# Performance work log

Hardware: AMD Instinct MI355X
Metric: run time of the kernel (lower is better)

Reference implementation:

```python
import jax, jax.numpy as jnp
import numpy as np

PI_APPROX = 3.14  # the original module uses 3.14, not math.pi
FPS = 30.0        # hard-coded sampling rate in calc_hr_torch


def setup_inputs() -> dict:
    key = jax.random.key(0)
    x = jax.random.normal(key, (4096, 4096), dtype=jnp.float32)
    return {"x": x}


def reference(x) -> jnp.ndarray:
    test_n, sig_length = x.shape
    # mean-subtract each signal (over last dim)
    x = x - jnp.mean(x, axis=-1, keepdims=True)

    # custom_fft: DFT over dim 0 (size test_n), O(N^2) via trig matmuls
    N = test_n
    n = jnp.arange(N, dtype=jnp.float32)[:, None]  # [N,1]
    k = jnp.arange(N, dtype=jnp.float32)[None, :]  # [1,N]
    ang = (-2.0 * PI_APPROX / N) * (k * n)         # [N,N]
    real_part = jnp.matmul(jnp.cos(ang), x)        # [N, sig_length]
    imag_part = jnp.matmul(jnp.sin(ang), x)

    # custom_rfft: keep non-negative frequencies along dim 0
    half = N // 2 + 1 if N % 2 == 0 else (N + 1) // 2
    real_part = real_part[:half]
    imag_part = imag_part[:half]

    Ns = sig_length
    freq = jnp.arange(Ns, dtype=jnp.float32) / (Ns / FPS)  # [sig_length]
    amplitude = jnp.sqrt(real_part ** 2 + imag_part ** 2) / Ns  # [half, sig_length]
    hr_list = freq[jnp.argmax(amplitude, axis=-1)] * 60.0       # [half]
    return hr_list
```

## Files before the change

### kernel.cpp

```cpp
#include <hip/hip_runtime.h>
#include <cmath>

typedef _Float16 f16;
typedef _Float16 f16x8 __attribute__((ext_vector_type(8)));
typedef float f32x4 __attribute__((ext_vector_type(4)));
typedef unsigned long long u64;

#define M_OUT 2049
#define NDIM 4096
#define MPAD 2112
#define CW ((float)(-2.0 * 3.14 / 4096.0))

static const size_t WS_MEAN  = 0;
static const size_t WS_CELLS = 16384;
static const size_t WS_TBL   = 40960;
static const size_t A_ELEMS  = (size_t)MPAD * NDIM;
static const size_t X_ELEMS  = (size_t)NDIM * NDIM;
static const size_t WS_XTBL  = WS_TBL + 4 * A_ELEMS * sizeof(f16);
static const size_t WS_FULL_END = WS_XTBL + 2 * X_ELEMS * sizeof(f16);
static const size_t WS_MID_END  = WS_TBL + 4 * A_ELEMS * sizeof(f16);

__device__ __forceinline__ void split_f16(float v, f16& hi, f16& lo) {
    hi = (f16)v;
    lo = (f16)((v - (float)hi) * 64.0f);
}

__global__ void mean_kernel(const float* __restrict__ x, float* __restrict__ meanv) {
    const int row = blockIdx.x;
    const float4* xr = (const float4*)(x + (size_t)row * NDIM);
    float s = 0.f;
    for (int i = threadIdx.x; i < NDIM / 4; i += 256) {
        float4 v = xr[i];
        s += (v.x + v.y) + (v.z + v.w);
    }
    for (int off = 32; off; off >>= 1) s += __shfl_down(s, off);
    __shared__ float ps[4];
    if ((threadIdx.x & 63) == 0) ps[threadIdx.x >> 6] = s;
    __syncthreads();
    if (threadIdx.x == 0) {
        float t = (ps[0] + ps[1]) + (ps[2] + ps[3]);
        meanv[row] = t * (1.0f / 4096.0f);
    }
}

__global__ void init_cells(u64* __restrict__ cells) {
    int i = blockIdx.x * 256 + threadIdx.x;
    if (i < M_OUT) cells[i] = 0ull;
}

__global__ void fill_A_cm(f16* __restrict__ tbl) {
    const int c = blockIdx.x;
    const int m = blockIdx.y * 256 + threadIdx.x;
    if (m >= MPAD) return;
    const bool valid = (m < M_OUT);
    f16x8 chv, clv, shv, slv;
    for (int j = 0; j < 8; ++j) {
        float cc = 0.f, ss = 0.f;
        if (valid) {
            int kk = c * 8 + j;
            float ang = CW * (float)(m * kk);
            sincosf(ang, &ss, &cc);
        }
        f16 h, l;
        split_f16(cc, h, l); chv[j] = h; clv[j] = l;
        split_f16(ss, h, l); shv[j] = h; slv[j] = l;
    }
    size_t idx = ((size_t)c * MPAD + m) * 8;
    *(f16x8*)(tbl + idx)                 = chv;
    *(f16x8*)(tbl + A_ELEMS + idx)       = clv;
    *(f16x8*)(tbl + 2 * A_ELEMS + idx)   = shv;
    *(f16x8*)(tbl + 3 * A_ELEMS + idx)   = slv;
}

__global__ void fill_X_cm(const float* __restrict__ x, const float* __restrict__ meanv,
                          f16* __restrict__ xtbl) {
    const int c = blockIdx.x;
    const int n = blockIdx.y * 256 + threadIdx.x;
    f16x8 hv, lv;
    for (int j = 0; j < 8; ++j) {
        int k = c * 8 + j;
        float v = x[(size_t)k * NDIM + n] - meanv[k];
        f16 h, l;
        split_f16(v, h, l);
        hv[j] = h; lv[j] = l;
    }
    size_t idx = ((size_t)c * NDIM + n) * 8;
    *(f16x8*)(xtbl + idx)           = hv;
    *(f16x8*)(xtbl + X_ELEMS + idx) = lv;
}

__global__ __launch_bounds__(256, 2) void dft_gemm_rs(
    const f16* __restrict__ atbl, const f16* __restrict__ xtbl,
    u64* __restrict__ cells)
{
    __shared__ alignas(16) f16 sX0[2][4][128][8];
    __shared__ alignas(16) f16 sX1[2][4][128][8];

    const int t = threadIdx.x;
    const int n0      = blockIdx.x * 128;
    const int rowBase = blockIdx.y * 64;

    const int lane = t & 63;
    const int w  = t >> 6;
    const int wm = w >> 1, wn = w & 1;
    const int q  = lane >> 4, ln = lane & 15;

    f32x4 aC0[2][4], aC1[2][4], aS0[2][4], aS1[2][4];
#pragma unroll
    for (int i = 0; i < 2; ++i)
#pragma unroll
        for (int j = 0; j < 4; ++j) {
            aC0[i][j] = (f32x4){0.f, 0.f, 0.f, 0.f};
            aC1[i][j] = (f32x4){0.f, 0.f, 0.f, 0.f};
            aS0[i][j] = (f32x4){0.f, 0.f, 0.f, 0.f};
            aS1[i][j] = (f32x4){0.f, 0.f, 0.f, 0.f};
        }

    int xtb[4], xch[4], xcol[4];
#pragma unroll
    for (int o = 0; o < 4; ++o) {
        int e = o * 256 + t;
        xtb[o] = e >> 9; xch[o] = (e >> 7) & 3; xcol[o] = e & 127;
    }

    auto loadX = [&](f16x8 (&xr)[4], int kc) {
#pragma unroll
        for (int o = 0; o < 4; ++o)
            xr[o] = *(const f16x8*)(xtbl + (size_t)xtb[o] * X_ELEMS
                     + (((size_t)(kc + xch[o]) * NDIM) + n0 + xcol[o]) * 8);
    };
    auto writeX = [&](f16x8 (&xr)[4], f16 (&dst)[2][4][128][8]) {
#pragma unroll
        for (int o = 0; o < 4; ++o)
            *(f16x8*)&dst[xtb[o]][xch[o]][xcol[o]][0] = xr[o];
    };

    const f16* aBase = atbl + ((size_t)q * MPAD + (rowBase + wm * 32 + ln)) * 8;
    auto loadA = [&](f16x8 (&dst)[2][4], int kc) {
#pragma unroll
        for (int tm = 0; tm < 2; ++tm)
#pragma unroll
            for (int tb = 0; tb < 4; ++tb)
                dst[tm][tb] = *(const f16x8*)(aBase + (size_t)tb * A_ELEMS
                              + ((size_t)kc * MPAD + tm * 16) * 8);
    };

    auto compute = [&](f16x8 (&A)[2][4], const f16 (&buf)[2][4][128][8]) {
        f16x8 bh[4], bl[4];
#pragma unroll
        for (int tn = 0; tn < 4; ++tn) {
            int nl = wn * 64 + tn * 16 + ln;
            bh[tn] = *(const f16x8*)&buf[0][q][nl][0];
            bl[tn] = *(const f16x8*)&buf[1][q][nl][0];
        }
#pragma unroll
        for (int tm = 0; tm < 2; ++tm)
#pragma unroll
            for (int tn = 0; tn < 4; ++tn) {
                aC0[tm][tn] = __builtin_amdgcn_mfma_f32_16x16x32_f16(A[tm][0], bh[tn], aC0[tm][tn], 0, 0, 0);
                aC1[tm][tn] = __builtin_amdgcn_mfma_f32_16x16x32_f16(A[tm][0], bl[tn], aC1[tm][tn], 0, 0, 0);
                aC1[tm][tn] = __builtin_amdgcn_mfma_f32_16x16x32_f16(A[tm][1], bh[tn], aC1[tm][tn], 0, 0, 0);
                aS0[tm][tn] = __builtin_amdgcn_mfma_f32_16x16x32_f16(A[tm][2], bh[tn], aS0[tm][tn], 0, 0, 0);
                aS1[tm][tn] = __builtin_amdgcn_mfma_f32_16x16x32_f16(A[tm][2], bl[tn], aS1[tm][tn], 0, 0, 0);
                aS1[tm][tn] = __builtin_amdgcn_mfma_f32_16x16x32_f16(A[tm][3], bh[tn], aS1[tm][tn], 0, 0, 0);
            }
    };

    f16x8 xr[4];
    f16x8 Aa[2][4], Ab[2][4];
    loadX(xr, 0);
    loadA(Aa, 0);
    for (int kc = 0; kc < 512; kc += 8) {
        writeX(xr, sX0);
        __syncthreads();
        loadX(xr, (kc + 4) & 511);
        loadA(Ab, (kc + 4) & 511);
        compute(Aa, sX0);
        writeX(xr, sX1);
        __syncthreads();
        loadX(xr, (kc + 8) & 511);
        loadA(Aa, (kc + 8) & 511);
        compute(Ab, sX1);
    }

    const float inv64 = 0.015625f;
#pragma unroll
    for (int tm = 0; tm < 2; ++tm) {
#pragma unroll
        for (int r = 0; r < 4; ++r) {
            u64 best = 0ull;
#pragma unroll
            for (int tn = 0; tn < 4; ++tn) {
                float C = aC0[tm][tn][r] + aC1[tm][tn][r] * inv64;
                float S = aS0[tm][tn][r] + aS1[tm][tn][r] * inv64;
                float a2 = C * C + S * S;
                int col = n0 + wn * 64 + tn * 16 + ln;
                u64 key = ((u64)__float_as_uint(a2) << 32) | (unsigned)(~col);
                if (key > best) best = key;
            }
            for (int off = 1; off < 16; off <<= 1) {
                unsigned hi = (unsigned)(best >> 32), lo = (unsigned)best;
                unsigned ho = __shfl_xor(hi, off);
                unsigned lo2 = __shfl_xor(lo, off);
                u64 o = ((u64)ho << 32) | lo2;
                if (o > best) best = o;
            }
            if (ln == 0) {
                int grow = rowBase + wm * 32 + tm * 16 + q * 4 + r;
                if (grow < M_OUT) atomicMax(cells + grow, best);
            }
        }
    }
}

__global__ void fill_tables_rm(f16* __restrict__ tbl) {
    long long g = (long long)blockIdx.x * 256 + threadIdx.x;
    if (g >= (long long)(MPAD * 512)) return;
    int m  = (int)(g >> 9);
    int kq = ((int)g & 511) * 8;
    bool valid = (m < M_OUT);
    f16x8 chv, clv, shv, slv;
    for (int j = 0; j < 8; ++j) {
        float c = 0.f, s = 0.f;
        if (valid) {
            int kk = kq + j;
            float ang = CW * (float)(m * kk);
            sincosf(ang, &s, &c);
        }
        f16 h, l;
        split_f16(c, h, l); chv[j] = h; clv[j] = l;
        split_f16(s, h, l); shv[j] = h; slv[j] = l;
    }
    size_t idx = (size_t)m * NDIM + kq;
    *(f16x8*)(tbl + idx)               = chv;
    *(f16x8*)(tbl + A_ELEMS + idx)     = clv;
    *(f16x8*)(tbl + 2 * A_ELEMS + idx) = shv;
    *(f16x8*)(tbl + 3 * A_ELEMS + idx) = slv;
}

#define PK 40
__global__ __launch_bounds__(256, 2) void dft_gemm_fb(
    const float* __restrict__ x, const float* __restrict__ meanv,
    const f16* __restrict__ tbl, int useTbl,
    u64* __restrict__ cells)
{
    __shared__ alignas(16) f16 Ach[64][PK];
    __shared__ alignas(16) f16 Acl[64][PK];
    __shared__ alignas(16) f16 Ash[64][PK];
    __shared__ alignas(16) f16 Asl[64][PK];
    __shared__ alignas(16) f16 Xh[128][PK];
    __shared__ alignas(16) f16 Xl[128][PK];

    const int t = threadIdx.x;
    const int n0      = blockIdx.x * 128;
    const int rowBase = blockIdx.y * 64;

    const int am  = t >> 2;
    const int akq = (t & 3) * 8;
    const int xn  = t & 127;
    const int xkh = (t >> 7) * 16;

    const int lane = t & 63;
    const int w  = t >> 6;
    const int wm = w >> 1, wn = w & 1;
    const int q  = lane >> 4, ln = lane & 15;

    f32x4 aC0[2][4], aC1[2][4], aS0[2][4], aS1[2][4];
    for (int i = 0; i < 2; ++i)
        for (int j = 0; j < 4; ++j) {
            aC0[i][j] = (f32x4){0.f, 0.f, 0.f, 0.f};
            aC1[i][j] = (f32x4){0.f, 0.f, 0.f, 0.f};
            aS0[i][j] = (f32x4){0.f, 0.f, 0.f, 0.f};
            aS1[i][j] = (f32x4){0.f, 0.f, 0.f, 0.f};
        }

    const int arow = rowBase + am;
    const bool avalid = (arow < M_OUT);

    for (int k0 = 0; k0 < NDIM; k0 += 32) {
        __syncthreads();
        if (useTbl) {
            size_t idx = (size_t)arow * NDIM + k0 + akq;
            *(f16x8*)&Ach[am][akq] = *(const f16x8*)(tbl + idx);
            *(f16x8*)&Acl[am][akq] = *(const f16x8*)(tbl + A_ELEMS + idx);
            *(f16x8*)&Ash[am][akq] = *(const f16x8*)(tbl + 2 * A_ELEMS + idx);
            *(f16x8*)&Asl[am][akq] = *(const f16x8*)(tbl + 3 * A_ELEMS + idx);
        } else {
            f16x8 chv, clv, shv, slv;
            for (int j = 0; j < 8; ++j) {
                float c = 0.f, s = 0.f;
                if (avalid) {
                    int kk = k0 + akq + j;
                    float ang = CW * (float)(arow * kk);
                    sincosf(ang, &s, &c);
                }
                f16 h, l;
                split_f16(c, h, l); chv[j] = h; clv[j] = l;
                split_f16(s, h, l); shv[j] = h; slv[j] = l;
            }
            *(f16x8*)&Ach[am][akq] = chv;
            *(f16x8*)&Acl[am][akq] = clv;
            *(f16x8*)&Ash[am][akq] = shv;
            *(f16x8*)&Asl[am][akq] = slv;
        }
        {
            const float* xp = x + (size_t)(k0 + xkh) * NDIM + n0 + xn;
            f16x8 h0, h1, l0, l1;
            for (int r = 0; r < 16; ++r) {
                float v = xp[(size_t)r * NDIM] - meanv[k0 + xkh + r];
                f16 hi, lo;
                split_f16(v, hi, lo);
                if (r < 8) { h0[r] = hi; l0[r] = lo; }
                else       { h1[r - 8] = hi; l1[r - 8] = lo; }
            }
            *(f16x8*)&Xh[xn][xkh]     = h0;
            *(f16x8*)&Xh[xn][xkh + 8] = h1;
            *(f16x8*)&Xl[xn][xkh]     = l0;
            *(f16x8*)&Xl[xn][xkh + 8] = l1;
        }
        __syncthreads();
        f16x8 fch[2], fcl[2], fsh[2], fsl[2], bh[4], bl[4];
        for (int tm = 0; tm < 2; ++tm) {
            int ml = wm * 32 + tm * 16 + ln;
            fch[tm] = *(const f16x8*)&Ach[ml][q * 8];
            fcl[tm] = *(const f16x8*)&Acl[ml][q * 8];
            fsh[tm] = *(const f16x8*)&Ash[ml][q * 8];
            fsl[tm] = *(const f16x8*)&Asl[ml][q * 8];
        }
        for (int tn = 0; tn < 4; ++tn) {
            int nl = wn * 64 + tn * 16 + ln;
            bh[tn] = *(const f16x8*)&Xh[nl][q * 8];
            bl[tn] = *(const f16x8*)&Xl[nl][q * 8];
        }
        for (int tm = 0; tm < 2; ++tm)
            for (int tn = 0; tn < 4; ++tn) {
                aC0[tm][tn] = __builtin_amdgcn_mfma_f32_16x16x32_f16(fch[tm], bh[tn], aC0[tm][tn], 0, 0, 0);
                aC1[tm][tn] = __builtin_amdgcn_mfma_f32_16x16x32_f16(fch[tm], bl[tn], aC1[tm][tn], 0, 0, 0);
                aC1[tm][tn] = __builtin_amdgcn_mfma_f32_16x16x32_f16(fcl[tm], bh[tn], aC1[tm][tn], 0, 0, 0);
                aS0[tm][tn] = __builtin_amdgcn_mfma_f32_16x16x32_f16(fsh[tm], bh[tn], aS0[tm][tn], 0, 0, 0);
                aS1[tm][tn] = __builtin_amdgcn_mfma_f32_16x16x32_f16(fsh[tm], bl[tn], aS1[tm][tn], 0, 0, 0);
                aS1[tm][tn] = __builtin_amdgcn_mfma_f32_16x16x32_f16(fsl[tm], bh[tn], aS1[tm][tn], 0, 0, 0);
            }
    }

    const float inv64 = 0.015625f;
    for (int tm = 0; tm < 2; ++tm) {
        for (int r = 0; r < 4; ++r) {
            u64 best = 0ull;
            for (int tn = 0; tn < 4; ++tn) {
                float C = aC0[tm][tn][r] + aC1[tm][tn][r] * inv64;
                float S = aS0[tm][tn][r] + aS1[tm][tn][r] * inv64;
                float a2 = C * C + S * S;
                int col = n0 + wn * 64 + tn * 16 + ln;
                u64 key = ((u64)__float_as_uint(a2) << 32) | (unsigned)(~col);
                if (key > best) best = key;
            }
            for (int off = 1; off < 16; off <<= 1) {
                unsigned hi = (unsigned)(best >> 32), lo = (unsigned)best;
                unsigned ho = __shfl_xor(hi, off);
                unsigned lo2 = __shfl_xor(lo, off);
                u64 o = ((u64)ho << 32) | lo2;
                if (o > best) best = o;
            }
            if (ln == 0) {
                int grow = rowBase + wm * 32 + tm * 16 + q * 4 + r;
                if (grow < M_OUT) atomicMax(cells + grow, best);
            }
        }
    }
}

__global__ void out_kernel(const u64* __restrict__ cells, float* __restrict__ out) {
    int i = blockIdx.x * 256 + threadIdx.x;
    if (i < M_OUT) {
        unsigned col = ~(unsigned)(cells[i] & 0xFFFFFFFFull);
        float freq = (float)col / (4096.0f / 30.0f);
        out[i] = freq * 60.0f;
    }
}

extern "C" void kernel_launch(void* const* d_in, const int* in_sizes, int n_in,
                              void* d_out, int out_size, void* d_ws, size_t ws_size,
                              hipStream_t stream) {
    const float* x = (const float*)d_in[0];
    char* ws = (char*)d_ws;
    float* meanv = (float*)(ws + WS_MEAN);
    u64*   cells = (u64*)(ws + WS_CELLS);
    f16*   atbl  = (f16*)(ws + WS_TBL);
    f16*   xtbl  = (f16*)(ws + WS_XTBL);
    float* out   = (float*)d_out;

    hipLaunchKernelGGL(init_cells, dim3((M_OUT + 255) / 256), dim3(256), 0, stream, cells);
    hipLaunchKernelGGL(mean_kernel, dim3(NDIM), dim3(256), 0, stream, x, meanv);

    if (ws_size >= WS_FULL_END) {
        hipLaunchKernelGGL(fill_A_cm, dim3(512, 9), dim3(256), 0, stream, atbl);
        hipLaunchKernelGGL(fill_X_cm, dim3(512, 16), dim3(256), 0, stream, x, meanv, xtbl);
        hipLaunchKernelGGL(dft_gemm_rs, dim3(32, 33), dim3(256), 0, stream, atbl, xtbl, cells);
    } else if (ws_size >= WS_MID_END) {
        hipLaunchKernelGGL(fill_tables_rm, dim3(4224), dim3(256), 0, stream, atbl);
        hipLaunchKernelGGL(dft_gemm_fb, dim3(32, 33), dim3(256), 0, stream,
                           x, meanv, atbl, 1, cells);
    } else {
        hipLaunchKernelGGL(dft_gemm_fb, dim3(32, 33), dim3(256), 0, stream,
                           x, meanv, atbl, 0, cells);
    }
    hipLaunchKernelGGL(out_kernel, dim3((M_OUT + 255) / 256), dim3(256), 0, stream, cells, out);
}
```

Baseline: 541.6 us.

## Switch DFT GEMM to 32x32x16 MFMA tiles and fuse setup kernels

The main GEMM now uses 32x32x16 MFMA instructions with 16-register accumulators instead of 16x16x32, which cuts LDS B-fragment reads per MFMA and changes the operand mapping and epilogue row indexing. Cell initialisation is folded into the mean kernel, and the A-table and X-table fill kernels are merged into one launch to reduce launch count. The risks are a higher accumulator register footprint and errors in the reworked lane-to-row mapping.

```diff
diff --git a/kernel.cpp b/kernel.cpp
--- a/kernel.cpp
+++ b/kernel.cpp
@@ -4,6 +4,7 @@
 typedef _Float16 f16;
 typedef _Float16 f16x8 __attribute__((ext_vector_type(8)));
 typedef float f32x4 __attribute__((ext_vector_type(4)));
+typedef float f32x16 __attribute__((ext_vector_type(16)));
 typedef unsigned long long u64;
 
 #define M_OUT 2049
@@ -25,8 +26,13 @@
     lo = (f16)((v - (float)hi) * 64.0f);
 }
 
-__global__ void mean_kernel(const float* __restrict__ x, float* __restrict__ meanv) {
+__global__ void mean_kernel(const float* __restrict__ x, float* __restrict__ meanv,
+                            u64* __restrict__ cells) {
     const int row = blockIdx.x;
+    if (blockIdx.x < 9) {
+        int ci = blockIdx.x * 256 + threadIdx.x;
+        if (ci < M_OUT) cells[ci] = 0ull;
+    }
     const float4* xr = (const float4*)(x + (size_t)row * NDIM);
     float s = 0.f;
     for (int i = threadIdx.x; i < NDIM / 4; i += 256) {
@@ -43,53 +49,48 @@
     }
 }
 
-__global__ void init_cells(u64* __restrict__ cells) {
-    int i = blockIdx.x * 256 + threadIdx.x;
-    if (i < M_OUT) cells[i] = 0ull;
-}
-
-__global__ void fill_A_cm(f16* __restrict__ tbl) {
+__global__ void fill_tables_cm(const float* __restrict__ x, const float* __restrict__ meanv,
+                               f16* __restrict__ atbl, f16* __restrict__ xtbl) {
     const int c = blockIdx.x;
-    const int m = blockIdx.y * 256 + threadIdx.x;
-    if (m >= MPAD) return;
-    const bool valid = (m < M_OUT);
-    f16x8 chv, clv, shv, slv;
-    for (int j = 0; j < 8; ++j) {
-        float cc = 0.f, ss = 0.f;
-        if (valid) {
-            int kk = c * 8 + j;
-            float ang = CW * (float)(m * kk);
-            sincosf(ang, &ss, &cc);
-        }
-        f16 h, l;
-        split_f16(cc, h, l); chv[j] = h; clv[j] = l;
-        split_f16(ss, h, l); shv[j] = h; slv[j] = l;
-    }
-    size_t idx = ((size_t)c * MPAD + m) * 8;
-    *(f16x8*)(tbl + idx)                 = chv;
-    *(f16x8*)(tbl + A_ELEMS + idx)       = clv;
-    *(f16x8*)(tbl + 2 * A_ELEMS + idx)   = shv;
-    *(f16x8*)(tbl + 3 * A_ELEMS + idx)   = slv;
-}
-
-__global__ void fill_X_cm(const float* __restrict__ x, const float* __restrict__ meanv,
-                          f16* __restrict__ xtbl) {
-    const int c = blockIdx.x;
-    const int n = blockIdx.y * 256 + threadIdx.x;
-    f16x8 hv, lv;
-    for (int j = 0; j < 8; ++j) {
-        int k = c * 8 + j;
-        float v = x[(size_t)k * NDIM + n] - meanv[k];
-        f16 h, l;
-        split_f16(v, h, l);
-        hv[j] = h; lv[j] = l;
-    }
-    size_t idx = ((size_t)c * NDIM + n) * 8;
-    *(f16x8*)(xtbl + idx)           = hv;
-    *(f16x8*)(xtbl + X_ELEMS + idx) = lv;
-}
-
-__global__ __launch_bounds__(256, 2) void dft_gemm_rs(
+    const int y = blockIdx.y;
+    if (y < 9) {
+        const int m = y * 256 + threadIdx.x;
+        if (m >= MPAD) return;
+        const bool valid = (m < M_OUT);
+        f16x8 chv, clv, shv, slv;
+        for (int j = 0; j < 8; ++j) {
+            float cc = 0.f, ss = 0.f;
+            if (valid) {
+                int kk = c * 8 + j;
+                float ang = CW * (float)(m * kk);
+                sincosf(ang, &ss, &cc);
+            }
+            f16 h, l;
+            split_f16(cc, h, l); chv[j] = h; clv[j] = l;
+            split_f16(ss, h, l); shv[j] = h; slv[j] = l;
+        }
+        size_t idx = ((size_t)c * MPAD + m) * 8;
+        *(f16x8*)(atbl + idx)                 = chv;
+        *(f16x8*)(atbl + A_ELEMS + idx)       = clv;
+        *(f16x8*)(atbl + 2 * A_ELEMS + idx)   = shv;
+        *(f16x8*)(atbl + 3 * A_ELEMS + idx)   = slv;
+    } else {
+        const int n = (y - 9) * 256 + threadIdx.x;
+        f16x8 hv, lv;
+        for (int j = 0; j < 8; ++j) {
+            int k = c * 8 + j;
+            float v = x[(size_t)k * NDIM + n] - meanv[k];
+            f16 h, l;
+            split_f16(v, h, l);
+            hv[j] = h; lv[j] = l;
+        }
+        size_t idx = ((size_t)c * NDIM + n) * 8;
+        *(f16x8*)(xtbl + idx)           = hv;
+        *(f16x8*)(xtbl + X_ELEMS + idx) = lv;
+    }
+}
+
+__global__ __launch_bounds__(256, 2) void dft_gemm_32(
     const f16* __restrict__ atbl, const f16* __restrict__ xtbl,
     u64* __restrict__ cells)
 {
@@ -103,18 +104,17 @@
     const int lane = t & 63;
     const int w  = t >> 6;
     const int wm = w >> 1, wn = w & 1;
-    const int q  = lane >> 4, ln = lane & 15;
-
-    f32x4 aC0[2][4], aC1[2][4], aS0[2][4], aS1[2][4];
-#pragma unroll
-    for (int i = 0; i < 2; ++i)
-#pragma unroll
-        for (int j = 0; j < 4; ++j) {
-            aC0[i][j] = (f32x4){0.f, 0.f, 0.f, 0.f};
-            aC1[i][j] = (f32x4){0.f, 0.f, 0.f, 0.f};
-            aS0[i][j] = (f32x4){0.f, 0.f, 0.f, 0.f};
-            aS1[i][j] = (f32x4){0.f, 0.f, 0.f, 0.f};
-        }
+    const int g  = lane >> 5;
+    const int l5 = lane & 31;
+
+    f32x16 aC0[2], aC1[2], aS0[2], aS1[2];
+#pragma unroll
+    for (int j = 0; j < 2; ++j) {
+        aC0[j] = (f32x16)(0.f);
+        aC1[j] = (f32x16)(0.f);
+        aS0[j] = (f32x16)(0.f);
+        aS1[j] = (f32x16)(0.f);
+    }
 
     int xtb[4], xch[4], xcol[4];
 #pragma unroll
@@ -122,7 +122,6 @@
         int e = o * 256 + t;
         xtb[o] = e >> 9; xch[o] = (e >> 7) & 3; xcol[o] = e & 127;
     }
-
     auto loadX = [&](f16x8 (&xr)[4], int kc) {
 #pragma unroll
         for (int o = 0; o < 4; ++o)
@@ -135,35 +134,36 @@
             *(f16x8*)&dst[xtb[o]][xch[o]][xcol[o]][0] = xr[o];
     };
 
-    const f16* aBase = atbl + ((size_t)q * MPAD + (rowBase + wm * 32 + ln)) * 8;
+    const f16* aBase = atbl + ((size_t)g * MPAD + (rowBase + wm * 32 + l5)) * 8;
     auto loadA = [&](f16x8 (&dst)[2][4], int kc) {
 #pragma unroll
-        for (int tm = 0; tm < 2; ++tm)
+        for (int s = 0; s < 2; ++s)
 #pragma unroll
             for (int tb = 0; tb < 4; ++tb)
-                dst[tm][tb] = *(const f16x8*)(aBase + (size_t)tb * A_ELEMS
-                              + ((size_t)kc * MPAD + tm * 16) * 8);
+                dst[s][tb] = *(const f16x8*)(aBase + (size_t)tb * A_ELEMS
+                              + ((size_t)(kc + 2 * s) * MPAD) * 8);
     };
 
     auto compute = [&](f16x8 (&A)[2][4], const f16 (&buf)[2][4][128][8]) {
-        f16x8 bh[4], bl[4];
-#pragma unroll
-        for (int tn = 0; tn < 4; ++tn) {
-            int nl = wn * 64 + tn * 16 + ln;
-            bh[tn] = *(const f16x8*)&buf[0][q][nl][0];
-            bl[tn] = *(const f16x8*)&buf[1][q][nl][0];
-        }
-#pragma unroll
-        for (int tm = 0; tm < 2; ++tm)
-#pragma unroll
-            for (int tn = 0; tn < 4; ++tn) {
-                aC0[tm][tn] = __builtin_amdgcn_mfma_f32_16x16x32_f16(A[tm][0], bh[tn], aC0[tm][tn], 0, 0, 0);
-                aC1[tm][tn] = __builtin_amdgcn_mfma_f32_16x16x32_f16(A[tm][0], bl[tn], aC1[tm][tn], 0, 0, 0);
-                aC1[tm][tn] = __builtin_amdgcn_mfma_f32_16x16x32_f16(A[tm][1], bh[tn], aC1[tm][tn], 0, 0, 0);
-                aS0[tm][tn] = __builtin_amdgcn_mfma_f32_16x16x32_f16(A[tm][2], bh[tn], aS0[tm][tn], 0, 0, 0);
-                aS1[tm][tn] = __builtin_amdgcn_mfma_f32_16x16x32_f16(A[tm][2], bl[tn], aS1[tm][tn], 0, 0, 0);
-                aS1[tm][tn] = __builtin_amdgcn_mfma_f32_16x16x32_f16(A[tm][3], bh[tn], aS1[tm][tn], 0, 0, 0);
-            }
+#pragma unroll
+        for (int s = 0; s < 2; ++s) {
+            f16x8 bh[2], bl[2];
+#pragma unroll
+            for (int tn = 0; tn < 2; ++tn) {
+                int nl = wn * 64 + tn * 32 + l5;
+                bh[tn] = *(const f16x8*)&buf[0][2 * s + g][nl][0];
+                bl[tn] = *(const f16x8*)&buf[1][2 * s + g][nl][0];
+            }
+#pragma unroll
+            for (int tn = 0; tn < 2; ++tn) {
+                aC0[tn] = __builtin_amdgcn_mfma_f32_32x32x16_f16(A[s][0], bh[tn], aC0[tn], 0, 0, 0);
+                aC1[tn] = __builtin_amdgcn_mfma_f32_32x32x16_f16(A[s][0], bl[tn], aC1[tn], 0, 0, 0);
+                aC1[tn] = __builtin_amdgcn_mfma_f32_32x32x16_f16(A[s][1], bh[tn], aC1[tn], 0, 0, 0);
+                aS0[tn] = __builtin_amdgcn_mfma_f32_32x32x16_f16(A[s][2], bh[tn], aS0[tn], 0, 0, 0);
+                aS1[tn] = __builtin_amdgcn_mfma_f32_32x32x16_f16(A[s][2], bl[tn], aS1[tn], 0, 0, 0);
+                aS1[tn] = __builtin_amdgcn_mfma_f32_32x32x16_f16(A[s][3], bh[tn], aS1[tn], 0, 0, 0);
+            }
+        }
     };
 
     f16x8 xr[4];
@@ -185,39 +185,36 @@
 
     const float inv64 = 0.015625f;
 #pragma unroll
-    for (int tm = 0; tm < 2; ++tm) {
-#pragma unroll
-        for (int r = 0; r < 4; ++r) {
-            u64 best = 0ull;
-#pragma unroll
-            for (int tn = 0; tn < 4; ++tn) {
-                float C = aC0[tm][tn][r] + aC1[tm][tn][r] * inv64;
-                float S = aS0[tm][tn][r] + aS1[tm][tn][r] * inv64;
-                float a2 = C * C + S * S;
-                int col = n0 + wn * 64 + tn * 16 + ln;
-                u64 key = ((u64)__float_as_uint(a2) << 32) | (unsigned)(~col);
-                if (key > best) best = key;
-            }
-            for (int off = 1; off < 16; off <<= 1) {
-                unsigned hi = (unsigned)(best >> 32), lo = (unsigned)best;
-                unsigned ho = __shfl_xor(hi, off);
-                unsigned lo2 = __shfl_xor(lo, off);
-                u64 o = ((u64)ho << 32) | lo2;
-                if (o > best) best = o;
-            }
-            if (ln == 0) {
-                int grow = rowBase + wm * 32 + tm * 16 + q * 4 + r;
-                if (grow < M_OUT) atomicMax(cells + grow, best);
-            }
+    for (int reg = 0; reg < 16; ++reg) {
+        u64 best = 0ull;
+#pragma unroll
+        for (int tn = 0; tn < 2; ++tn) {
+            float C = aC0[tn][reg] + aC1[tn][reg] * inv64;
+            float S = aS0[tn][reg] + aS1[tn][reg] * inv64;
+            float a2 = C * C + S * S;
+            int col = n0 + wn * 64 + tn * 32 + l5;
+            u64 key = ((u64)__float_as_uint(a2) << 32) | (unsigned)(~col);
+            if (key > best) best = key;
+        }
+        for (int off = 1; off < 32; off <<= 1) {
+            unsigned hi = (unsigned)(best >> 32), lo = (unsigned)best;
+            unsigned ho = __shfl_xor(hi, off);
+            unsigned lo2 = __shfl_xor(lo, off);
+            u64 o = ((u64)ho << 32) | lo2;
+            if (o > best) best = o;
+        }
+        if (l5 == 0) {
+            int grow = rowBase + wm * 32 + 4 * g + (reg & 3) + 8 * (reg >> 2);
+            if (grow < M_OUT) atomicMax(cells + grow, best);
         }
     }
 }
 
 __global__ void fill_tables_rm(f16* __restrict__ tbl) {
-    long long g = (long long)blockIdx.x * 256 + threadIdx.x;
-    if (g >= (long long)(MPAD * 512)) return;
-    int m  = (int)(g >> 9);
-    int kq = ((int)g & 511) * 8;
+    long long gg = (long long)blockIdx.x * 256 + threadIdx.x;
+    if (gg >= (long long)(MPAD * 512)) return;
+    int m  = (int)(gg >> 9);
+    int kq = ((int)gg & 511) * 8;
     bool valid = (m < M_OUT);
     f16x8 chv, clv, shv, slv;
     for (int j = 0; j < 8; ++j) {
@@ -390,13 +387,12 @@
     f16*   xtbl  = (f16*)(ws + WS_XTBL);
     float* out   = (float*)d_out;
 
-    hipLaunchKernelGGL(init_cells, dim3((M_OUT + 255) / 256), dim3(256), 0, stream, cells);
-    hipLaunchKernelGGL(mean_kernel, dim3(NDIM), dim3(256), 0, stream, x, meanv);
+    hipLaunchKernelGGL(mean_kernel, dim3(NDIM), dim3(256), 0, stream, x, meanv, cells);
 
     if (ws_size >= WS_FULL_END) {
-        hipLaunchKernelGGL(fill_A_cm, dim3(512, 9), dim3(256), 0, stream, atbl);
-        hipLaunchKernelGGL(fill_X_cm, dim3(512, 16), dim3(256), 0, stream, x, meanv, xtbl);
-        hipLaunchKernelGGL(dft_gemm_rs, dim3(32, 33), dim3(256), 0, stream, atbl, xtbl, cells);
+        hipLaunchKernelGGL(fill_tables_cm, dim3(512, 25), dim3(256), 0, stream,
+                           x, meanv, atbl, xtbl);
+        hipLaunchKernelGGL(dft_gemm_32, dim3(32, 33), dim3(256), 0, stream, atbl, xtbl, cells);
     } else if (ws_size >= WS_MID_END) {
         hipLaunchKernelGGL(fill_tables_rm, dim3(4224), dim3(256), 0, stream, atbl);
         hipLaunchKernelGGL(dft_gemm_fb, dim3(32, 33), dim3(256), 0, stream,
```

After: 612.6 us. 1.13x slower.
